# Kernel tuning notes

Hardware: AMD Instinct MI355X
Metric: run time of the kernel (lower is better)

Reference implementation:

```python
import jax, jax.numpy as jnp
import numpy as np

DIM_IN = 512
DIM_HEAD = 64
HEADS = 8
KV_HEADS = 2
CONTEXT_LEN = 4096
B, N = 4, 2048


def setup_inputs() -> dict:
    key = jax.random.key(0)
    ks = jax.random.split(key, 6)
    s = 1.0 / np.sqrt(DIM_IN)
    return {
        "x": jax.random.normal(ks[0], (B, DIM_IN, N), dtype=jnp.float32),
        "gamma": jnp.ones((DIM_IN,), jnp.float32),
        "beta": jnp.zeros((DIM_IN,), jnp.float32),
        "Wq": jax.random.normal(ks[1], (DIM_IN, DIM_HEAD * HEADS), jnp.float32) * s,
        "Wkv": jax.random.normal(ks[2], (DIM_IN, DIM_HEAD * KV_HEADS * 2), jnp.float32) * s,
        "Wout": jax.random.normal(ks[3], (DIM_HEAD * HEADS, DIM_IN), jnp.float32) * (1.0 / np.sqrt(DIM_HEAD * HEADS)),
        "bout": jnp.zeros((DIM_IN,), jnp.float32),
    }


def _rotate_half(t):
    t1, t2 = jnp.split(t, 2, axis=-1)
    return jnp.concatenate([-t2, t1], axis=-1)


def _xpos_rotary(q, k, n, dim_head, scale_base):
    # lucidrains-style xPos rotary embedding
    pos = jnp.arange(n, dtype=jnp.float32)
    inv_freq = 1.0 / (10000.0 ** (jnp.arange(0, dim_head, 2, dtype=jnp.float32) / dim_head))
    freqs = pos[:, None] * inv_freq[None, :]            # (n, dh/2)
    freqs = jnp.concatenate([freqs, freqs], axis=-1)    # (n, dh)
    base_scale = (jnp.arange(0, dim_head, 2, dtype=jnp.float32) + 0.4 * dim_head) / (1.4 * dim_head)
    power = (pos - n // 2) / scale_base                 # (n,)
    scale = base_scale[None, :] ** power[:, None]       # (n, dh/2)
    scale = jnp.concatenate([scale, scale], axis=-1)    # (n, dh)
    cos, sin = jnp.cos(freqs), jnp.sin(freqs)
    q = (q * cos + _rotate_half(q) * sin) * scale
    k = (k * cos + _rotate_half(k) * sin) / scale
    return q, k


def reference(x, gamma, beta, Wq, Wkv, Wout, bout):
    b, d, n = x.shape
    h, kvh, dh = HEADS, KV_HEADS, DIM_HEAD
    xt = jnp.swapaxes(x, 1, 2)                           # (b, n, d)
    mu = jnp.mean(xt, axis=-1, keepdims=True)
    var = jnp.mean((xt - mu) ** 2, axis=-1, keepdims=True)
    xn = (xt - mu) * jax.lax.rsqrt(var + 1e-5) * gamma + beta
    q = (xn @ Wq).reshape(b, n, h, dh).transpose(0, 2, 1, 3)      # (b, h, n, dh)
    kv = xn @ Wkv
    k, v = jnp.split(kv, 2, axis=-1)
    k = k.reshape(b, n, kvh, dh).transpose(0, 2, 1, 3)            # (b, kvh, n, dh)
    v = v.reshape(b, n, kvh, dh).transpose(0, 2, 1, 3)
    r = h // kvh
    # repeat 'b h n d -> b (r h) n d': tile whole kv-head block r times
    k = jnp.tile(k, (1, r, 1, 1))
    v = jnp.tile(v, (1, r, 1, 1))
    q, k = _xpos_rotary(q, k, n, dh, CONTEXT_LEN)
    scores = jnp.einsum("bhqd,bhkd->bhqk", q, k) * (1.0 / np.sqrt(dh))
    attn = jax.nn.softmax(scores, axis=-1)
    out = jnp.einsum("bhqk,bhkd->bhqd", attn, v)                  # (b, h, n, dh)
    out = out.transpose(0, 2, 1, 3).reshape(b, n, h * dh)
    y = xn + out @ Wout + bout                                    # residual uses normed x
    return jnp.swapaxes(y, 1, 2)                                  # (b, d, n)
```

## Files before the change

kernel.cpp:

```cpp
#include <hip/hip_runtime.h>
#include <stdint.h>

#define DIM 512
#define DH  64
#define NH  8
#define NKV 2
#define NB  4
#define NS  2048
#define TAB (NS*32)

typedef __attribute__((ext_vector_type(8))) short short8;
typedef __attribute__((ext_vector_type(4))) short s16x4;
typedef __attribute__((ext_vector_type(4))) float f32x4;
typedef __attribute__((ext_vector_type(16))) float f32x16;
typedef __attribute__((ext_vector_type(2))) unsigned uint2v;
typedef __attribute__((ext_vector_type(4))) unsigned uint4v;

__device__ __forceinline__ unsigned short f2bf(float f) {
  union { float f; unsigned u; } v; v.f = f;
  return (unsigned short)((v.u + 0x7fffu + ((v.u >> 16) & 1u)) >> 16);
}
__device__ __forceinline__ float bf2f(unsigned short b) {
  union { unsigned u; float f; } v; v.u = ((unsigned)b) << 16;
  return v.f;
}
__device__ __forceinline__ unsigned cvt_pk_bf16(float a, float b) {
  unsigned r;
  asm("v_cvt_pk_bf16_f32 %0, %1, %2" : "=v"(r) : "v"(a), "v"(b));
  return r;
}
__device__ __forceinline__ float exp2_raw(float x) {
  float r;
  asm("v_exp_f32 %0, %1" : "=v"(r) : "v"(x));
  return r;
}
__device__ __forceinline__ float rcp_raw(float x) {
  float r;
  asm("v_rcp_f32 %0, %1" : "=v"(r) : "v"(x));
  return r;
}
__device__ __forceinline__ short8 merge8(short8 a, short8 b, float rl) {
  uint4v u;
  #pragma unroll
  for (int i = 0; i < 4; ++i) {
    float x0 = (bf2f((unsigned short)a[2*i])   + bf2f((unsigned short)b[2*i]))   * rl;
    float x1 = (bf2f((unsigned short)a[2*i+1]) + bf2f((unsigned short)b[2*i+1])) * rl;
    u[i] = cvt_pk_bf16(x0, x1);
  }
  return __builtin_bit_cast(short8, u);
}

__global__ __launch_bounds__(256) void lnprep_kernel(const float* __restrict__ x,
    const float* __restrict__ gamma, const float* __restrict__ beta,
    const float* __restrict__ Wq, const float* __restrict__ Wkv, const float* __restrict__ Wout,
    unsigned short* __restrict__ xn, unsigned short* __restrict__ Wqkvt,
    unsigned short* __restrict__ Woutt, float* __restrict__ tabs) {
  __shared__ float t[64][65];
  const int gid = blockIdx.x;
  const int tid = threadIdx.x;
  if (gid < 256) {
    const int b = gid >> 6;
    const int n0 = (gid & 63) * 32;
    const int nl = tid & 31, grp = tid >> 5;
    const float* xb = x + (size_t)b * DIM * NS + (size_t)grp * 64 * NS + n0 + nl;
    float v[64];
    float s = 0.f, s2 = 0.f;
    #pragma unroll
    for (int i = 0; i < 64; ++i) {
      v[i] = xb[(size_t)i * NS];
      s += v[i]; s2 += v[i] * v[i];
    }
    float* sm = &t[0][0];
    float* sq = &t[8][0];
    float* mu_s = &t[16][0];
    float* rs_s = &t[17][0];
    sm[grp*32 + nl] = s; sq[grp*32 + nl] = s2;
    __syncthreads();
    if (tid < 32) {
      float ts = 0.f, ts2 = 0.f;
      #pragma unroll
      for (int g = 0; g < 8; ++g) { ts += sm[g*32 + tid]; ts2 += sq[g*32 + tid]; }
      float mu = ts * (1.f/512.f);
      float var = ts2 * (1.f/512.f) - mu*mu;
      mu_s[tid] = mu; rs_s[tid] = rsqrtf(var + 1e-5f);
    }
    __syncthreads();
    const float mu = mu_s[nl], rs = rs_s[nl];
    unsigned short* dst = &xn[((size_t)(b*NS + n0 + nl))*DIM + grp*64];
    #pragma unroll
    for (int c = 0; c < 8; ++c) {
      short8 o;
      #pragma unroll
      for (int j = 0; j < 8; ++j) {
        int d = grp*64 + c*8 + j;
        o[j] = (short)f2bf((v[c*8 + j] - mu) * rs * gamma[d] + beta[d]);
      }
      *(short8*)&dst[c*8] = o;
    }
    return;
  }
  const int id = gid - 256;
  if (id >= 160) {
    int base = (id - 160) * 256 + tid;
    #pragma unroll 4
    for (int ii = 0; ii < 32; ++ii) {
      int tix = base + ii * 2048;
      int pos = tix >> 5, i = tix & 31;
      float inv = exp2f(-(float)i * (13.287712379549449f / 32.f));
      float ang = (float)pos * inv;
      float sv, cv; sincosf(ang, &sv, &cv);
      float bse = ((float)(2*i) + 25.6f) / 89.6f;
      float power = ((float)pos - 1024.f) / 4096.f;
      float sc = exp2f(power * log2f(bse));
      tabs[tix]         = cv;
      tabs[TAB + tix]   = sv;
      tabs[2*TAB + tix] = sc * 0.125f * 1.4426950408889634f;
      tabs[3*TAB + tix] = 1.f / sc;
    }
    return;
  }
  const float* src; int W, k0, c0; unsigned short* dst; int drow0;
  if (id < 64)      { src = Wq;  W = 512; k0 = (id>>3)*64;        c0 = (id&7)*64;        dst = Wqkvt; drow0 = c0; }
  else if (id < 96) { int i2 = id-64; src = Wkv; W = 256; k0 = (i2>>2)*64; c0 = (i2&3)*64; dst = Wqkvt; drow0 = 512 + c0; }
  else              { int i3 = id-96; src = Wout; W = 512; k0 = (i3>>3)*64; c0 = (i3&7)*64; dst = Woutt; drow0 = c0; }
  #pragma unroll 4
  for (int it = 0; it < 16; ++it) {
    int row = it*4 + (tid>>6), col = tid & 63;
    t[row][col] = src[(size_t)(k0+row)*W + c0 + col];
  }
  __syncthreads();
  #pragma unroll 4
  for (int it = 0; it < 16; ++it) {
    int row = it*4 + (tid>>6), col = tid & 63;
    dst[(size_t)(drow0 + row)*512 + k0 + col] = f2bf(t[col][row]);
  }
}

__global__ __launch_bounds__(256, 3) void qkv_kernel(const unsigned short* __restrict__ A,
    const unsigned short* __restrict__ Bt, const float* __restrict__ tabs,
    unsigned short* __restrict__ q, unsigned short* __restrict__ k,
    unsigned short* __restrict__ v) {
  __shared__ __align__(16) short As[2][64][40];
  __shared__ __align__(16) short Bs[2][128][40];
  const int m0 = blockIdx.x * 64, ntile = blockIdx.y, n0 = ntile * 128;
  const int tid = threadIdx.x, w = tid >> 6, lane = tid & 63;
  const int wr = w >> 1, wc = w & 1;
  f32x4 acc[2][4];
  #pragma unroll
  for (int i = 0; i < 2; ++i)
    #pragma unroll
    for (int j = 0; j < 4; ++j) acc[i][j] = (f32x4){0.f,0.f,0.f,0.f};
  const int rA = tid >> 2, c8 = (tid & 3) * 8;
  const unsigned short* Ar0 = &A[(size_t)(m0 + rA)*DIM + c8];
  const unsigned short* Br0 = &Bt[(size_t)(n0 + rA)*DIM + c8];
  const unsigned short* Br1 = &Bt[(size_t)(n0 + 64 + rA)*DIM + c8];
  *(short8*)&As[0][rA][c8]      = *(const short8*)Ar0;
  *(short8*)&Bs[0][rA][c8]      = *(const short8*)Br0;
  *(short8*)&Bs[0][64 + rA][c8] = *(const short8*)Br1;
  short8 pa0 = *(const short8*)(Ar0 + 32);
  short8 pb0 = *(const short8*)(Br0 + 32);
  short8 pb1 = *(const short8*)(Br1 + 32);
  __syncthreads();
  for (int t = 0; t < 16; ++t) {
    const int cur = t & 1;
    short8 af[2], bfr[4];
    #pragma unroll
    for (int mf = 0; mf < 2; ++mf)
      af[mf] = *(const short8*)&As[cur][wr*32 + mf*16 + (lane & 15)][(lane >> 4)*8];
    #pragma unroll
    for (int nf = 0; nf < 4; ++nf)
      bfr[nf] = *(const short8*)&Bs[cur][wc*64 + nf*16 + (lane & 15)][(lane >> 4)*8];
    __builtin_amdgcn_s_setprio(1);
    #pragma unroll
    for (int mf = 0; mf < 2; ++mf)
      #pragma unroll
      for (int nf = 0; nf < 4; ++nf)
        acc[mf][nf] = __builtin_amdgcn_mfma_f32_16x16x32_bf16(af[mf], bfr[nf], acc[mf][nf], 0, 0, 0);
    __builtin_amdgcn_s_setprio(0);
    if (t < 15) {
      *(short8*)&As[cur^1][rA][c8]      = pa0;
      *(short8*)&Bs[cur^1][rA][c8]      = pb0;
      *(short8*)&Bs[cur^1][64 + rA][c8] = pb1;
      if (t < 14) {
        const int kc = (t + 2) * 32;
        pa0 = *(const short8*)(Ar0 + kc);
        pb0 = *(const short8*)(Br0 + kc);
        pb1 = *(const short8*)(Br1 + kc);
      }
      __syncthreads();
    }
  }
  const int mw = m0 + wr*32, cw = n0 + wc*64;
  if (ntile < 4) {
    #pragma unroll
    for (int nfp = 0; nfp < 2; ++nfp) {
      const int c_lo = cw + nfp*16 + (lane & 15);
      const int head = c_lo >> 6, ii = c_lo & 31;
      const float* tb = tabs + ii;
      #pragma unroll
      for (int mf = 0; mf < 2; ++mf) {
        #pragma unroll
        for (int r = 0; r < 4; ++r) {
          int mm = mw + mf*16 + (lane >> 4)*4 + r;
          int bb = mm >> 11, n = mm & (NS-1);
          float cv = tb[n*32], sv = tb[TAB + n*32], qs = tb[2*TAB + n*32];
          float lo = acc[mf][nfp][r], hi = acc[mf][nfp+2][r];
          size_t base = (((size_t)bb*NH + head)*NS + n)*DH;
          q[base + ii]      = f2bf((lo*cv - hi*sv)*qs);
          q[base + ii + 32] = f2bf((hi*cv + lo*sv)*qs);
        }
      }
    }
  } else if (ntile == 4) {
    #pragma unroll
    for (int nfp = 0; nfp < 2; ++nfp) {
      const int c_lo = cw + nfp*16 + (lane & 15);
      const int kvh = (c_lo - 512) >> 6, ii = c_lo & 31;
      const float* tb = tabs + ii;
      #pragma unroll
      for (int mf = 0; mf < 2; ++mf) {
        #pragma unroll
        for (int r = 0; r < 4; ++r) {
          int mm = mw + mf*16 + (lane >> 4)*4 + r;
          int bb = mm >> 11, n = mm & (NS-1);
          float cv = tb[n*32], sv = tb[TAB + n*32], ks = tb[3*TAB + n*32];
          float lo = acc[mf][nfp][r], hi = acc[mf][nfp+2][r];
          size_t base = (((size_t)bb*NKV + kvh)*NS + n)*DH;
          k[base + ii]      = f2bf((lo*cv - hi*sv)*ks);
          k[base + ii + 32] = f2bf((hi*cv + lo*sv)*ks);
        }
      }
    }
  } else {
    #pragma unroll
    for (int nf = 0; nf < 4; ++nf) {
      const int c = cw + nf*16 + (lane & 15);
      const int rel = c - 640;
      const int kvh = rel >> 6, dd = rel & 63;
      #pragma unroll
      for (int mf = 0; mf < 2; ++mf) {
        int mm = mw + mf*16 + (lane >> 4)*4;
        int bb = mm >> 11, n = mm & (NS-1);
        s16x4 sv4;
        #pragma unroll
        for (int r = 0; r < 4; ++r) sv4[r] = (short)f2bf(acc[mf][nf][r]);
        *(s16x4*)&v[(((size_t)bb*NKV + kvh)*DH + dd)*NS + n] = sv4;
      }
    }
  }
}

__global__ __launch_bounds__(256, 4) void attn_kernel(const unsigned short* __restrict__ q,
    const unsigned short* __restrict__ kg, const unsigned short* __restrict__ vtp,
    unsigned short* __restrict__ op0, unsigned short* __restrict__ op1,
    float* __restrict__ lp) {
  __shared__ __align__(16) short kt[2][64][72];
  __shared__ __align__(16) short vt[2][64][72];
  const int bid = blockIdx.x;
  const int dsr = (bid & 7) * 128 + (bid >> 3);
  const int qt   = dsr & 15;
  const int half = (dsr >> 4) & 1;
  const int bh   = dsr >> 5;
  const int h = bh & 7, b = bh >> 3;
  const int kvh = h & (NKV-1);
  const int q0 = qt * 128;
  const int tid = threadIdx.x, w = tid >> 6, lane = tid & 63;
  const int l31 = lane & 31, hf = lane >> 5;
  short8 q8[4];
  const unsigned short* qp = q + (((size_t)b*NH + h)*NS + q0 + w*32 + l31)*DH + hf*8;
  #pragma unroll
  for (int s = 0; s < 4; ++s) q8[s] = *(const short8*)(qp + s*16);
  const unsigned short* kb = kg + ((size_t)b*NKV + kvh)*NS*DH;
  const unsigned short* vb = vtp + ((size_t)b*NKV + kvh)*DH*NS;
  const int kbase = half * 1024;
  const int srow = tid >> 2, scol = (tid & 3) * 16;
  *(short8*)&kt[0][srow][scol]     = *(const short8*)&kb[(size_t)(kbase + srow)*DH + scol];
  *(short8*)&kt[0][srow][scol + 8] = *(const short8*)&kb[(size_t)(kbase + srow)*DH + scol + 8];
  *(short8*)&vt[0][srow][scol]     = *(const short8*)&vb[(size_t)srow*NS + kbase + scol];
  *(short8*)&vt[0][srow][scol + 8] = *(const short8*)&vb[(size_t)srow*NS + kbase + scol + 8];
  short8 kr0 = *(const short8*)&kb[(size_t)(kbase + 64 + srow)*DH + scol];
  short8 kr1 = *(const short8*)&kb[(size_t)(kbase + 64 + srow)*DH + scol + 8];
  short8 vr0 = *(const short8*)&vb[(size_t)srow*NS + kbase + 64 + scol];
  short8 vr1 = *(const short8*)&vb[(size_t)srow*NS + kbase + 64 + scol + 8];
  f32x16 o0 = {}, o1 = {};
  float lsum = 0.f;
  __syncthreads();
  for (int t = 0; t < 16; ++t) {
    const int cur = t & 1;
    short8 kf0[4], kf1[4];
    #pragma unroll
    for (int s = 0; s < 4; ++s) {
      kf0[s] = *(const short8*)&kt[cur][l31][s*16 + hf*8];
      kf1[s] = *(const short8*)&kt[cur][32 + l31][s*16 + hf*8];
    }
    f32x16 st0 = {}, st1 = {};
    __builtin_amdgcn_s_setprio(1);
    #pragma unroll
    for (int s = 0; s < 4; ++s) {
      st0 = __builtin_amdgcn_mfma_f32_32x32x16_bf16(kf0[s], q8[s], st0, 0, 0, 0);
      st1 = __builtin_amdgcn_mfma_f32_32x32x16_bf16(kf1[s], q8[s], st1, 0, 0, 0);
    }
    __builtin_amdgcn_s_setprio(0);
    float p0[16], p1[16];
    #pragma unroll
    for (int r = 0; r < 16; ++r) {
      p0[r] = exp2_raw(st0[r]);
      p1[r] = exp2_raw(st1[r]);
      lsum += p0[r] + p1[r];
    }
    short8 paf[4];
    #pragma unroll
    for (int t2 = 0; t2 < 2; ++t2) {
      const float* pp = t2 ? p1 : p0;
      #pragma unroll
      for (int w16 = 0; w16 < 2; ++w16) {
        const int rb = w16*8;
        unsigned x = cvt_pk_bf16(pp[rb+0], pp[rb+1]);
        unsigned z = cvt_pk_bf16(pp[rb+2], pp[rb+3]);
        unsigned y = cvt_pk_bf16(pp[rb+4], pp[rb+5]);
        unsigned u = cvt_pk_bf16(pp[rb+6], pp[rb+7]);
        uint2v r1 = __builtin_amdgcn_permlane32_swap(x, y, false, false);
        uint2v r2 = __builtin_amdgcn_permlane32_swap(z, u, false, false);
        uint4v pk4;
        pk4[0] = r1[0]; pk4[1] = r2[0]; pk4[2] = r1[1]; pk4[3] = r2[1];
        paf[t2*2 + w16] = __builtin_bit_cast(short8, pk4);
      }
    }
    __builtin_amdgcn_s_setprio(1);
    #pragma unroll
    for (int kwin = 0; kwin < 4; ++kwin) {
      short8 vf0 = *(const short8*)&vt[cur][l31][kwin*16 + hf*8];
      short8 vf1 = *(const short8*)&vt[cur][32 + l31][kwin*16 + hf*8];
      o0 = __builtin_amdgcn_mfma_f32_32x32x16_bf16(paf[kwin], vf0, o0, 0, 0, 0);
      o1 = __builtin_amdgcn_mfma_f32_32x32x16_bf16(paf[kwin], vf1, o1, 0, 0, 0);
    }
    __builtin_amdgcn_s_setprio(0);
    if (t < 15) {
      *(short8*)&kt[cur^1][srow][scol]     = kr0;
      *(short8*)&kt[cur^1][srow][scol + 8] = kr1;
      *(short8*)&vt[cur^1][srow][scol]     = vr0;
      *(short8*)&vt[cur^1][srow][scol + 8] = vr1;
      if (t < 14) {
        const int k2 = kbase + (t + 2) * 64;
        kr0 = *(const short8*)&kb[(size_t)(k2 + srow)*DH + scol];
        kr1 = *(const short8*)&kb[(size_t)(k2 + srow)*DH + scol + 8];
        vr0 = *(const short8*)&vb[(size_t)srow*NS + k2 + scol];
        vr1 = *(const short8*)&vb[(size_t)srow*NS + k2 + scol + 8];
      }
      __syncthreads();
    }
  }
  lsum += __shfl_xor(lsum, 32);
  if (hf == 0)
    lp[(size_t)half*NB*NH*NS + ((size_t)b*NH + h)*NS + q0 + w*32 + l31] = lsum;
  unsigned short* op = half ? op1 : op0;
  #pragma unroll
  for (int r = 0; r < 16; ++r) {
    const int ql = (r & 3) + 8*(r >> 2) + 4*hf;
    const int n = q0 + w*32 + ql;
    unsigned short* aor = &op[((size_t)b*NS + n)*DIM + h*DH + l31];
    aor[0]  = f2bf(o0[r]);
    aor[32] = f2bf(o1[r]);
  }
}

__global__ __launch_bounds__(256, 3) void out_kernel(const unsigned short* __restrict__ op0,
    const unsigned short* __restrict__ op1, const float* __restrict__ lp,
    const unsigned short* __restrict__ Bt, const unsigned short* __restrict__ xn,
    const float* __restrict__ bout, float* __restrict__ out) {
  __shared__ __align__(16) short As[2][64][40];
  __shared__ __align__(16) short Bs[2][128][40];
  const int m0 = blockIdx.x * 64, n0 = blockIdx.y * 128;
  const int tid = threadIdx.x, w = tid >> 6, lane = tid & 63;
  const int wr = w >> 1, wc = w & 1;
  f32x4 acc[2][4];
  #pragma unroll
  for (int i = 0; i < 2; ++i)
    #pragma unroll
    for (int j = 0; j < 4; ++j) acc[i][j] = (f32x4){0.f,0.f,0.f,0.f};
  const int rA = tid >> 2, c8 = (tid & 3) * 8;
  const int rowm = m0 + rA;
  const int b0 = rowm >> 11, nn0 = rowm & (NS-1);
  const float* lp0 = lp + ((size_t)b0*NH)*NS + nn0;
  const float* lp1 = lp0 + (size_t)NB*NH*NS;
  const unsigned short* A0 = &op0[(size_t)rowm*DIM + c8];
  const unsigned short* A1 = &op1[(size_t)rowm*DIM + c8];
  const unsigned short* Br0 = &Bt[(size_t)(n0 + rA)*DIM + c8];
  const unsigned short* Br1 = &Bt[(size_t)(n0 + 64 + rA)*DIM + c8];
  float rlc = rcp_raw(lp0[0] + lp1[0]);
  *(short8*)&As[0][rA][c8]      = merge8(*(const short8*)A0, *(const short8*)A1, rlc);
  *(short8*)&Bs[0][rA][c8]      = *(const short8*)Br0;
  *(short8*)&Bs[0][64 + rA][c8] = *(const short8*)Br1;
  short8 pa0 = *(const short8*)(A0 + 32);
  short8 pa1 = *(const short8*)(A1 + 32);
  float rlp = rlc;
  short8 pb0 = *(const short8*)(Br0 + 32);
  short8 pb1 = *(const short8*)(Br1 + 32);
  __syncthreads();
  for (int t = 0; t < 16; ++t) {
    const int cur = t & 1;
    short8 af[2], bfr[4];
    #pragma unroll
    for (int mf = 0; mf < 2; ++mf)
      af[mf] = *(const short8*)&As[cur][wr*32 + mf*16 + (lane & 15)][(lane >> 4)*8];
    #pragma unroll
    for (int nf = 0; nf < 4; ++nf)
      bfr[nf] = *(const short8*)&Bs[cur][wc*64 + nf*16 + (lane & 15)][(lane >> 4)*8];
    __builtin_amdgcn_s_setprio(1);
    #pragma unroll
    for (int mf = 0; mf < 2; ++mf)
      #pragma unroll
      for (int nf = 0; nf < 4; ++nf)
        acc[mf][nf] = __builtin_amdgcn_mfma_f32_16x16x32_bf16(af[mf], bfr[nf], acc[mf][nf], 0, 0, 0);
    __builtin_amdgcn_s_setprio(0);
    if (t < 15) {
      *(short8*)&As[cur^1][rA][c8]      = merge8(pa0, pa1, rlp);
      *(short8*)&Bs[cur^1][rA][c8]      = pb0;
      *(short8*)&Bs[cur^1][64 + rA][c8] = pb1;
      if (t < 14) {
        const int kc = (t + 2) * 32;
        pa0 = *(const short8*)(A0 + kc);
        pa1 = *(const short8*)(A1 + kc);
        pb0 = *(const short8*)(Br0 + kc);
        pb1 = *(const short8*)(Br1 + kc);
        const int h2 = (t + 2) >> 1;
        rlp = rcp_raw(lp0[h2*NS] + lp1[h2*NS]);
      }
      __syncthreads();
    }
  }
  const int mw = m0 + wr*32, cw = n0 + wc*64;
  #pragma unroll
  for (int nf = 0; nf < 4; ++nf) {
    const int d = cw + nf*16 + (lane & 15);
    const float bo = bout[d];
    #pragma unroll
    for (int mf = 0; mf < 2; ++mf) {
      const int mb = mw + mf*16 + (lane >> 4)*4;
      const int bb = mb >> 11, n = mb & (NS-1);
      f32x4 res;
      #pragma unroll
      for (int r = 0; r < 4; ++r)
        res[r] = acc[mf][nf][r] + bf2f(xn[(size_t)(mb + r)*DIM + d]) + bo;
      *(f32x4*)&out[((size_t)bb*DIM + d)*NS + n] = res;
    }
  }
}

extern "C" void kernel_launch(void* const* d_in, const int* in_sizes, int n_in,
                              void* d_out, int out_size, void* d_ws, size_t ws_size,
                              hipStream_t stream) {
  (void)in_sizes; (void)n_in; (void)out_size; (void)ws_size;
  const float* x     = (const float*)d_in[0];
  const float* gamma = (const float*)d_in[1];
  const float* beta  = (const float*)d_in[2];
  const float* Wq    = (const float*)d_in[3];
  const float* Wkv   = (const float*)d_in[4];
  const float* Wout  = (const float*)d_in[5];
  const float* bout  = (const float*)d_in[6];
  float* out = (float*)d_out;
  char* ws = (char*)d_ws;
  unsigned short* xn    = (unsigned short*)(ws);
  unsigned short* qb    = (unsigned short*)(ws + (size_t)(8<<20));
  unsigned short* kb    = (unsigned short*)(ws + (size_t)(16<<20));
  unsigned short* vb    = (unsigned short*)(ws + (size_t)(18<<20));
  unsigned short* op0   = (unsigned short*)(ws + (size_t)(20<<20));
  unsigned short* op1   = (unsigned short*)(ws + (size_t)(28<<20));
  unsigned short* wqkvt = (unsigned short*)(ws + (size_t)(36<<20));
  unsigned short* woutt = (unsigned short*)(ws + (size_t)(36<<20) + 786432);
  float* tabs           = (float*)(ws + (size_t)(36<<20) + 786432 + 524288);
  float* lp             = (float*)(ws + (size_t)(36<<20) + 786432 + 524288 + 1048576);

  lnprep_kernel<<<dim3(424), dim3(256), 0, stream>>>(x, gamma, beta, Wq, Wkv, Wout,
                                                     xn, wqkvt, woutt, tabs);
  qkv_kernel<<<dim3(128, 6), dim3(256), 0, stream>>>(xn, wqkvt, tabs, qb, kb, vb);
  attn_kernel<<<dim3(1024), dim3(256), 0, stream>>>(qb, kb, vb, op0, op1, lp);
  out_kernel<<<dim3(128, 4), dim3(256), 0, stream>>>(op0, op1, lp, woutt, xn, bout, out);
}
```

Before: 89.48 us.

## Process two query sub-tiles per warp in attention and swizzle QKV block order

Each attention warp now handles 64 query rows, split into two 32-row sub-tiles, instead of 32. Every K/V tile loaded into shared memory is therefore reused across twice as many queries, which halves the grid and the K/V traffic. The QK and softmax work of one sub-tile is interleaved with the PV MFMAs of the other so the exp work overlaps matrix work. The QKV GEMM grid is flattened and remapped into a per-XCD swizzled order. The costs are higher register pressure (the occupancy hint is dropped from launch bounds) and fewer blocks to fill the GPU.

```diff
diff --git a/kernel.cpp b/kernel.cpp
--- a/kernel.cpp
+++ b/kernel.cpp
@@ -48,6 +48,33 @@
     u[i] = cvt_pk_bf16(x0, x1);
   }
   return __builtin_bit_cast(short8, u);
+}
+__device__ __forceinline__ void softmax_frags(const f32x16& st0, const f32x16& st1,
+                                              float& lsum, short8* paf) {
+  float p0[16], p1[16];
+  #pragma unroll
+  for (int r = 0; r < 16; ++r) {
+    p0[r] = exp2_raw(st0[r]);
+    p1[r] = exp2_raw(st1[r]);
+    lsum += p0[r] + p1[r];
+  }
+  #pragma unroll
+  for (int t2 = 0; t2 < 2; ++t2) {
+    const float* pp = t2 ? p1 : p0;
+    #pragma unroll
+    for (int w16 = 0; w16 < 2; ++w16) {
+      const int rb = w16*8;
+      unsigned x = cvt_pk_bf16(pp[rb+0], pp[rb+1]);
+      unsigned z = cvt_pk_bf16(pp[rb+2], pp[rb+3]);
+      unsigned y = cvt_pk_bf16(pp[rb+4], pp[rb+5]);
+      unsigned u = cvt_pk_bf16(pp[rb+6], pp[rb+7]);
+      uint2v r1 = __builtin_amdgcn_permlane32_swap(x, y, false, false);
+      uint2v r2 = __builtin_amdgcn_permlane32_swap(z, u, false, false);
+      uint4v pk4;
+      pk4[0] = r1[0]; pk4[1] = r2[0]; pk4[2] = r1[1]; pk4[3] = r2[1];
+      paf[t2*2 + w16] = __builtin_bit_cast(short8, pk4);
+    }
+  }
 }
 
 __global__ __launch_bounds__(256) void lnprep_kernel(const float* __restrict__ x,
@@ -142,7 +169,10 @@
     unsigned short* __restrict__ v) {
   __shared__ __align__(16) short As[2][64][40];
   __shared__ __align__(16) short Bs[2][128][40];
-  const int m0 = blockIdx.x * 64, ntile = blockIdx.y, n0 = ntile * 128;
+  const int p = blockIdx.x;
+  const int dsr = (p & 7) * 96 + (p >> 3);
+  const int mt = dsr / 6, ntile = dsr - mt * 6;
+  const int m0 = mt * 64, n0 = ntile * 128;
   const int tid = threadIdx.x, w = tid >> 6, lane = tid & 63;
   const int wr = w >> 1, wc = w & 1;
   f32x4 acc[2][4];
@@ -250,26 +280,29 @@
   }
 }
 
-__global__ __launch_bounds__(256, 4) void attn_kernel(const unsigned short* __restrict__ q,
+__global__ __launch_bounds__(256) void attn_kernel(const unsigned short* __restrict__ q,
     const unsigned short* __restrict__ kg, const unsigned short* __restrict__ vtp,
     unsigned short* __restrict__ op0, unsigned short* __restrict__ op1,
     float* __restrict__ lp) {
   __shared__ __align__(16) short kt[2][64][72];
   __shared__ __align__(16) short vt[2][64][72];
   const int bid = blockIdx.x;
-  const int dsr = (bid & 7) * 128 + (bid >> 3);
-  const int qt   = dsr & 15;
-  const int half = (dsr >> 4) & 1;
-  const int bh   = dsr >> 5;
+  const int dsr = (bid & 7) * 64 + (bid >> 3);
+  const int qt   = dsr & 7;
+  const int half = (dsr >> 3) & 1;
+  const int bh   = dsr >> 4;
   const int h = bh & 7, b = bh >> 3;
   const int kvh = h & (NKV-1);
-  const int q0 = qt * 128;
+  const int q0 = qt * 256;
   const int tid = threadIdx.x, w = tid >> 6, lane = tid & 63;
   const int l31 = lane & 31, hf = lane >> 5;
-  short8 q8[4];
-  const unsigned short* qp = q + (((size_t)b*NH + h)*NS + q0 + w*32 + l31)*DH + hf*8;
-  #pragma unroll
-  for (int s = 0; s < 4; ++s) q8[s] = *(const short8*)(qp + s*16);
+  short8 qA[4], qB[4];
+  const unsigned short* qpA = q + (((size_t)b*NH + h)*NS + q0 + w*64 + l31)*DH + hf*8;
+  #pragma unroll
+  for (int s = 0; s < 4; ++s) {
+    qA[s] = *(const short8*)(qpA + s*16);
+    qB[s] = *(const short8*)(qpA + 32*DH + s*16);
+  }
   const unsigned short* kb = kg + ((size_t)b*NKV + kvh)*NS*DH;
   const unsigned short* vb = vtp + ((size_t)b*NKV + kvh)*DH*NS;
   const int kbase = half * 1024;
@@ -282,8 +315,8 @@
   short8 kr1 = *(const short8*)&kb[(size_t)(kbase + 64 + srow)*DH + scol + 8];
   short8 vr0 = *(const short8*)&vb[(size_t)srow*NS + kbase + 64 + scol];
   short8 vr1 = *(const short8*)&vb[(size_t)srow*NS + kbase + 64 + scol + 8];
-  f32x16 o0 = {}, o1 = {};
-  float lsum = 0.f;
+  f32x16 oA0 = {}, oA1 = {}, oB0 = {}, oB1 = {};
+  float lsA = 0.f, lsB = 0.f;
   __syncthreads();
   for (int t = 0; t < 16; ++t) {
     const int cur = t & 1;
@@ -293,46 +326,39 @@
       kf0[s] = *(const short8*)&kt[cur][l31][s*16 + hf*8];
       kf1[s] = *(const short8*)&kt[cur][32 + l31][s*16 + hf*8];
     }
-    f32x16 st0 = {}, st1 = {};
+    f32x16 stA0 = {}, stA1 = {};
     __builtin_amdgcn_s_setprio(1);
     #pragma unroll
     for (int s = 0; s < 4; ++s) {
-      st0 = __builtin_amdgcn_mfma_f32_32x32x16_bf16(kf0[s], q8[s], st0, 0, 0, 0);
-      st1 = __builtin_amdgcn_mfma_f32_32x32x16_bf16(kf1[s], q8[s], st1, 0, 0, 0);
+      stA0 = __builtin_amdgcn_mfma_f32_32x32x16_bf16(kf0[s], qA[s], stA0, 0, 0, 0);
+      stA1 = __builtin_amdgcn_mfma_f32_32x32x16_bf16(kf1[s], qA[s], stA1, 0, 0, 0);
     }
     __builtin_amdgcn_s_setprio(0);
-    float p0[16], p1[16];
-    #pragma unroll
-    for (int r = 0; r < 16; ++r) {
-      p0[r] = exp2_raw(st0[r]);
-      p1[r] = exp2_raw(st1[r]);
-      lsum += p0[r] + p1[r];
-    }
-    short8 paf[4];
-    #pragma unroll
-    for (int t2 = 0; t2 < 2; ++t2) {
-      const float* pp = t2 ? p1 : p0;
-      #pragma unroll
-      for (int w16 = 0; w16 < 2; ++w16) {
-        const int rb = w16*8;
-        unsigned x = cvt_pk_bf16(pp[rb+0], pp[rb+1]);
-        unsigned z = cvt_pk_bf16(pp[rb+2], pp[rb+3]);
-        unsigned y = cvt_pk_bf16(pp[rb+4], pp[rb+5]);
-        unsigned u = cvt_pk_bf16(pp[rb+6], pp[rb+7]);
-        uint2v r1 = __builtin_amdgcn_permlane32_swap(x, y, false, false);
-        uint2v r2 = __builtin_amdgcn_permlane32_swap(z, u, false, false);
-        uint4v pk4;
-        pk4[0] = r1[0]; pk4[1] = r2[0]; pk4[2] = r1[1]; pk4[3] = r2[1];
-        paf[t2*2 + w16] = __builtin_bit_cast(short8, pk4);
-      }
-    }
+    short8 pafA[4];
+    softmax_frags(stA0, stA1, lsA, pafA);
+    f32x16 stB0 = {}, stB1 = {};
     __builtin_amdgcn_s_setprio(1);
     #pragma unroll
+    for (int s = 0; s < 4; ++s) {
+      stB0 = __builtin_amdgcn_mfma_f32_32x32x16_bf16(kf0[s], qB[s], stB0, 0, 0, 0);
+      stB1 = __builtin_amdgcn_mfma_f32_32x32x16_bf16(kf1[s], qB[s], stB1, 0, 0, 0);
+    }
+    short8 vfr0[4], vfr1[4];
+    #pragma unroll
     for (int kwin = 0; kwin < 4; ++kwin) {
-      short8 vf0 = *(const short8*)&vt[cur][l31][kwin*16 + hf*8];
-      short8 vf1 = *(const short8*)&vt[cur][32 + l31][kwin*16 + hf*8];
-      o0 = __builtin_amdgcn_mfma_f32_32x32x16_bf16(paf[kwin], vf0, o0, 0, 0, 0);
-      o1 = __builtin_amdgcn_mfma_f32_32x32x16_bf16(paf[kwin], vf1, o1, 0, 0, 0);
+      vfr0[kwin] = *(const short8*)&vt[cur][l31][kwin*16 + hf*8];
+      vfr1[kwin] = *(const short8*)&vt[cur][32 + l31][kwin*16 + hf*8];
+      oA0 = __builtin_amdgcn_mfma_f32_32x32x16_bf16(pafA[kwin], vfr0[kwin], oA0, 0, 0, 0);
+      oA1 = __builtin_amdgcn_mfma_f32_32x32x16_bf16(pafA[kwin], vfr1[kwin], oA1, 0, 0, 0);
+    }
+    __builtin_amdgcn_s_setprio(0);
+    short8 pafB[4];
+    softmax_frags(stB0, stB1, lsB, pafB);
+    __builtin_amdgcn_s_setprio(1);
+    #pragma unroll
+    for (int kwin = 0; kwin < 4; ++kwin) {
+      oB0 = __builtin_amdgcn_mfma_f32_32x32x16_bf16(pafB[kwin], vfr0[kwin], oB0, 0, 0, 0);
+      oB1 = __builtin_amdgcn_mfma_f32_32x32x16_bf16(pafB[kwin], vfr1[kwin], oB1, 0, 0, 0);
     }
     __builtin_amdgcn_s_setprio(0);
     if (t < 15) {
@@ -350,17 +376,24 @@
       __syncthreads();
     }
   }
-  lsum += __shfl_xor(lsum, 32);
-  if (hf == 0)
-    lp[(size_t)half*NB*NH*NS + ((size_t)b*NH + h)*NS + q0 + w*32 + l31] = lsum;
+  lsA += __shfl_xor(lsA, 32);
+  lsB += __shfl_xor(lsB, 32);
+  float* lph = lp + (size_t)half*NB*NH*NS + ((size_t)b*NH + h)*NS;
+  if (hf == 0) {
+    lph[q0 + w*64 + l31]      = lsA;
+    lph[q0 + w*64 + 32 + l31] = lsB;
+  }
   unsigned short* op = half ? op1 : op0;
   #pragma unroll
   for (int r = 0; r < 16; ++r) {
     const int ql = (r & 3) + 8*(r >> 2) + 4*hf;
-    const int n = q0 + w*32 + ql;
-    unsigned short* aor = &op[((size_t)b*NS + n)*DIM + h*DH + l31];
-    aor[0]  = f2bf(o0[r]);
-    aor[32] = f2bf(o1[r]);
+    const int nA = q0 + w*64 + ql;
+    unsigned short* aorA = &op[((size_t)b*NS + nA)*DIM + h*DH + l31];
+    aorA[0]  = f2bf(oA0[r]);
+    aorA[32] = f2bf(oA1[r]);
+    unsigned short* aorB = &op[((size_t)b*NS + nA + 32)*DIM + h*DH + l31];
+    aorB[0]  = f2bf(oB0[r]);
+    aorB[32] = f2bf(oB1[r]);
   }
 }
 
@@ -473,7 +506,7 @@
 
   lnprep_kernel<<<dim3(424), dim3(256), 0, stream>>>(x, gamma, beta, Wq, Wkv, Wout,
                                                      xn, wqkvt, woutt, tabs);
-  qkv_kernel<<<dim3(128, 6), dim3(256), 0, stream>>>(xn, wqkvt, tabs, qb, kb, vb);
-  attn_kernel<<<dim3(1024), dim3(256), 0, stream>>>(qb, kb, vb, op0, op1, lp);
+  qkv_kernel<<<dim3(768), dim3(256), 0, stream>>>(xn, wqkvt, tabs, qb, kb, vb);
+  attn_kernel<<<dim3(512), dim3(256), 0, stream>>>(qb, kb, vb, op0, op1, lp);
   out_kernel<<<dim3(128, 4), dim3(256), 0, stream>>>(op0, op1, lp, woutt, xn, bout, out);
 }
```

Result: slower. 98.10 us (+9.6%).
